# Optimization experiments

Measured on AMD Instinct MI355X. Metric: run time of the kernel, lower is better.

Reference implementation:

```python
import jax, jax.numpy as jnp
import numpy as np
from jax import lax

H = 1024        # hidden_size
V_IN = 32000    # input_size (source vocab)
V_OUT = 32000   # output_size (target vocab)
S = 128         # source sentence length
MAX_STEPS = 51  # decode loop bound (loop <= 50)
EOS = 2         # target_vocab['<eos>']


def _lstm_cell(x, h, c, W_ih, W_hh, b_ih, b_hh):
    # torch LSTMCell: gate order i, f, g, o
    gates = jnp.dot(W_ih, x) + b_ih + jnp.dot(W_hh, h) + b_hh  # [4H]
    i, f, g, o = jnp.split(gates, 4)
    i = jax.nn.sigmoid(i)
    f = jax.nn.sigmoid(f)
    g = jnp.tanh(g)
    o = jax.nn.sigmoid(o)
    c2 = f * c + i * g
    return o * jnp.tanh(c2), c2


def setup_inputs() -> dict:
    key = jax.random.key(0)
    ks = jax.random.split(key, 16)
    sc = 0.02
    p = {}
    p['src_ids'] = jax.random.randint(ks[0], (S,), 1, V_IN)
    emb_in = jax.random.normal(ks[1], (V_IN, H), jnp.float32) * sc
    p['embed_input'] = emb_in.at[0].set(0.0)  # padding_idx=0
    p['W_ih_e'] = jax.random.normal(ks[2], (4 * H, H), jnp.float32) * sc
    p['W_hh_e'] = jax.random.normal(ks[3], (4 * H, H), jnp.float32) * sc
    p['b_ih_e'] = jnp.zeros((4 * H,), jnp.float32)
    p['b_hh_e'] = jnp.zeros((4 * H,), jnp.float32)
    p['W_li'] = jax.random.normal(ks[4], (V_OUT, H), jnp.float32) * sc
    p['b_li'] = jnp.zeros((V_OUT,), jnp.float32)
    emb_t = jax.random.normal(ks[5], (V_OUT, H), jnp.float32) * sc
    p['embed_target'] = emb_t.at[0].set(0.0)  # padding_idx=0
    p['W_ih_d'] = jax.random.normal(ks[6], (4 * H, H), jnp.float32) * sc
    p['W_hh_d'] = jax.random.normal(ks[7], (4 * H, H), jnp.float32) * sc
    p['b_ih_d'] = jnp.zeros((4 * H,), jnp.float32)
    p['b_hh_d'] = jnp.zeros((4 * H,), jnp.float32)
    p['W_lt'] = jax.random.normal(ks[8], (V_OUT, H), jnp.float32) * sc
    p['b_lt'] = jnp.zeros((V_OUT,), jnp.float32)
    p['W_tl'] = jax.random.normal(ks[9], (H, 2 * H), jnp.float32) * sc
    p['b_tl'] = jnp.zeros((H,), jnp.float32)
    return p


def reference(src_ids, embed_input, W_ih_e, W_hh_e, b_ih_e, b_hh_e,
              W_li, b_li, embed_target, W_ih_d, W_hh_d, b_ih_d, b_hh_d,
              W_lt, b_lt, W_tl, b_tl):
    # ---- encoder: sequential LSTMCell over source tokens ----
    def enc_step(carry, tok):
        h, c = carry
        x = embed_input[tok]
        h2, c2 = _lstm_cell(x, h, c, W_ih_e, W_hh_e, b_ih_e, b_hh_e)
        return (h2, c2), h2

    h0 = jnp.zeros((H,), embed_input.dtype)
    (hs, cx), hs_all = lax.scan(enc_step, (h0, h0), src_ids)  # hs_all: [S,H]

    # first predicted word from final encoder state (argmax(softmax(z)) == argmax(z))
    wid0 = jnp.argmax(jnp.dot(W_li, hs) + b_li)
    tk0 = embed_target[wid0]
    ht, cx = _lstm_cell(tk0, hs, cx, W_ih_d, W_hh_d, b_ih_d, b_hh_d)

    # ---- greedy decode loop (fixed 51 steps, masked after <eos>) ----
    def dec_step(carry, _):
        wid, ht, cx, done = carry
        target_k = embed_target[wid]
        # dot-product attention over encoder states, softmax along source dim
        scores = jnp.dot(hs_all, ht)              # [S]
        a_t = jax.nn.softmax(scores)              # [S]
        d = jnp.dot(a_t, hs_all)                  # [H]
        concat = jnp.concatenate([d, ht])         # [2H]
        ht_new = jnp.tanh(jnp.dot(W_tl, concat) + b_tl)
        logits = jnp.dot(W_lt, ht_new) + b_lt     # [V_OUT]
        wid_new = jnp.argmax(logits)
        is_eos = wid_new == EOS
        out_tok = jnp.where(done | is_eos, -1, wid_new)  # -1 = not emitted
        ht2, cx2 = _lstm_cell(target_k, ht, cx, W_ih_d, W_hh_d, b_ih_d, b_hh_d)
        return (wid_new, ht2, cx2, done | is_eos), (out_tok, logits)

    done0 = wid0 == EOS
    _, (toks, logits) = lax.scan(dec_step, (wid0, ht, cx, done0), None, length=MAX_STEPS)
    return toks, logits  # toks: [51] emitted ids (-1 after eos), logits: [51, V_OUT]
```

## Files before the change

### kernel.cpp

```cpp
#include <hip/hip_runtime.h>
#include <float.h>
#include <math.h>

#define H      1024
#define SLEN   128
#define VOUT   32000
#define NSTEP  51
#define EOS_ID 2
#define NB     256
#define BT     1024
#define NWAVES 16
#define HROWS  4
#define LROWS  125
#define TOKS_OFF 51
#define QTAB_BYTES (LROWS*H)

typedef float fv4 __attribute__((ext_vector_type(4)));

struct Xch {
  unsigned long long h [2][H];
  unsigned long long ht[2][H];
  unsigned long long sc[2][SLEN];
  unsigned long long pv[2][NB];
};
__device__ Xch g_x;

__device__ __forceinline__ float wredsum(float v){
  v += __shfl_xor(v, 32, 64);
  v += __shfl_xor(v, 16, 64);
  v += __shfl_xor(v,  8, 64);
  v += __shfl_xor(v,  4, 64);
  v += __shfl_xor(v,  2, 64);
  v += __shfl_xor(v,  1, 64);
  return v;
}
__device__ __forceinline__ float wredmax(float v){
  v = fmaxf(v, __shfl_xor(v, 32, 64));
  v = fmaxf(v, __shfl_xor(v, 16, 64));
  v = fmaxf(v, __shfl_xor(v,  8, 64));
  v = fmaxf(v, __shfl_xor(v,  4, 64));
  v = fmaxf(v, __shfl_xor(v,  2, 64));
  v = fmaxf(v, __shfl_xor(v,  1, 64));
  return v;
}
__device__ __forceinline__ float sigm(float x){ return 1.0f/(1.0f+expf(-x)); }

__device__ __forceinline__ unsigned long long pollraw(const unsigned long long* p, unsigned tag){
  unsigned long long v = __hip_atomic_load(p, __ATOMIC_RELAXED, __HIP_MEMORY_SCOPE_AGENT);
  while((unsigned)(v & 0xffull) != tag){
    __builtin_amdgcn_s_sleep(1);
    v = __hip_atomic_load(p, __ATOMIC_RELAXED, __HIP_MEMORY_SCOPE_AGENT);
  }
  return v;
}
__device__ __forceinline__ float pollf(const unsigned long long* p, unsigned tag){
  return __uint_as_float((unsigned)(pollraw(p, tag) >> 32));
}
__device__ __forceinline__ void pubf(unsigned long long* p, float x, unsigned tag){
  __hip_atomic_store(p, (((unsigned long long)__float_as_uint(x))<<32) | (unsigned long long)tag,
                     __ATOMIC_RELAXED, __HIP_MEMORY_SCOPE_AGENT);
}
__device__ __forceinline__ void pubpv(unsigned long long* p, float v, int idx, unsigned tag){
  unsigned long long lo = (((unsigned long long)(unsigned)idx) << 8) | (unsigned long long)tag;
  __hip_atomic_store(p, (((unsigned long long)__float_as_uint(v))<<32) | lo,
                     __ATOMIC_RELAXED, __HIP_MEMORY_SCOPE_AGENT);
}

__device__ __forceinline__ float partdot(const float* __restrict__ a,
                                         const float* __restrict__ hp, int lane){
  const float4* a4 = (const float4*)a;
  const float4* h4 = (const float4*)hp;
  float s = 0.f;
#pragma unroll
  for(int k=0;k<4;k++){
    float4 x = a4[lane + 64*k];
    float4 y = h4[lane + 64*k];
    s = fmaf(x.x,y.x,s); s = fmaf(x.y,y.y,s);
    s = fmaf(x.z,y.z,s); s = fmaf(x.w,y.w,s);
  }
  return s;
}
__device__ __forceinline__ float partdot_nt(const float* __restrict__ a,
                                            const float* __restrict__ hp, int lane){
  const fv4* a4 = (const fv4*)a;
  const float4* h4 = (const float4*)hp;
  float s = 0.f;
#pragma unroll
  for(int k=0;k<4;k++){
    fv4 x = __builtin_nontemporal_load(a4 + lane + 64*k);
    float4 y = h4[lane + 64*k];
    s = fmaf(x.x,y.x,s); s = fmaf(x.y,y.y,s);
    s = fmaf(x.z,y.z,s); s = fmaf(x.w,y.w,s);
  }
  return s;
}

__device__ __forceinline__ float dotq(unsigned u, float4 hv, float acc){
  acc = fmaf((float)((int)(u<<24)>>24), hv.x, acc);
  acc = fmaf((float)((int)(u<<16)>>24), hv.y, acc);
  acc = fmaf((float)((int)(u<< 8)>>24), hv.z, acc);
  acc = fmaf((float)((int) u     >>24), hv.w, acc);
  return acc;
}

extern "C" __global__ void __launch_bounds__(BT)
nmt_kernel(const int* __restrict__ src_ids,
           const float* __restrict__ embed_input,
           const float* __restrict__ W_ih_e, const float* __restrict__ W_hh_e,
           const float* __restrict__ b_ih_e, const float* __restrict__ b_hh_e,
           const float* __restrict__ W_li,  const float* __restrict__ b_li,
           const float* __restrict__ embed_target,
           const float* __restrict__ W_ih_d, const float* __restrict__ W_hh_d,
           const float* __restrict__ b_ih_d, const float* __restrict__ b_hh_d,
           const float* __restrict__ W_lt,  const float* __restrict__ b_lt,
           const float* __restrict__ W_tl,  const float* __restrict__ b_tl,
           float* __restrict__ out)
{
  const int tid  = threadIdx.x;
  const int b    = blockIdx.x;
  const int w    = tid >> 6;
  const int lane = tid & 63;
  const int grow = (w>>2)*H + 4*b + (w&3);

  extern __shared__ __align__(16) char qmem[];
  uint4* qtab = (uint4*)qmem;

  __shared__ __align__(16) float hbuf[H];
  __shared__ __align__(16) float hsrow[H];
  __shared__ __align__(16) float htn_lds[H];
  __shared__ __align__(16) float xenc[SLEN][NWAVES];
  __shared__ __align__(16) float Mloc[HROWS][SLEN];
  __shared__ __align__(16) float sraw[SLEN];
  __shared__ __align__(16) float vloc[128];
  __shared__ __align__(16) float qrho[128];
  __shared__ __align__(16) float qinv[128];
  __shared__ __align__(16) float qbias[128];
  __shared__ int   rlist[128];
  __shared__ float gw4[4][4];
  __shared__ float c4[4];
  __shared__ float hn2[NWAVES];
  __shared__ float wred2[4];
  __shared__ float redv[NWAVES];
  __shared__ int   redi[NWAVES];
  __shared__ float gwhh_l[NWAVES];
  __shared__ int   wid_sh, done_sh;
  __shared__ float e_sh, rhomax_sh;
  __shared__ int   rcnt_sh;

#define PVPOLL47(TAG) do{                                                      \
    if(w>=4 && w<8){                                                           \
      unsigned long long v = pollraw(&g_x.pv[(TAG)&1][((w-4)<<6)+lane], (TAG));\
      float val = __uint_as_float((unsigned)(v>>32));                          \
      int   idx = (int)((unsigned)(v>>8) & 0xffffffu);                         \
      _Pragma("unroll")                                                        \
      for(int dd=32; dd>=1; dd>>=1){                                           \
        float ov=__shfl_xor(val,dd,64); int oi=__shfl_xor(idx,dd,64);          \
        if(ov>val || (ov==val && oi<idx)){ val=ov; idx=oi; }                   \
      }                                                                        \
      if(lane==0){ redv[w]=val; redi[w]=idx; }                                 \
    }                                                                          \
  }while(0)

  hbuf[tid] = 0.f;
  if(tid<4) c4[tid] = 0.f;
  __syncthreads();

  {
    const float4* wr = (const float4*)(W_ih_e + (size_t)grow*H);
    float4 w0=wr[lane], w1=wr[lane+64], w2=wr[lane+128], w3=wr[lane+192];
    const float bias = b_ih_e[grow] + b_hh_e[grow];
    for(int t=0;t<SLEN;t+=2){
      const float4* xr = (const float4*)(embed_input + (size_t)src_ids[t]*H);
      const float4* yr = (const float4*)(embed_input + (size_t)src_ids[t+1]*H);
      float4 x0=xr[lane], x1=xr[lane+64], x2=xr[lane+128], x3=xr[lane+192];
      float4 y0=yr[lane], y1=yr[lane+64], y2=yr[lane+128], y3=yr[lane+192];
      float s, u;
      s = w0.x*x0.x;        s = fmaf(w0.y,x0.y,s); s = fmaf(w0.z,x0.z,s); s = fmaf(w0.w,x0.w,s);
      u = w0.x*y0.x;        u = fmaf(w0.y,y0.y,u); u = fmaf(w0.z,y0.z,u); u = fmaf(w0.w,y0.w,u);
      s = fmaf(w1.x,x1.x,s); s = fmaf(w1.y,x1.y,s); s = fmaf(w1.z,x1.z,s); s = fmaf(w1.w,x1.w,s);
      u = fmaf(w1.x,y1.x,u); u = fmaf(w1.y,y1.y,u); u = fmaf(w1.z,y1.z,u); u = fmaf(w1.w,y1.w,u);
      s = fmaf(w2.x,x2.x,s); s = fmaf(w2.y,x2.y,s); s = fmaf(w2.z,x2.z,s); s = fmaf(w2.w,x2.w,s);
      u = fmaf(w2.x,y2.x,u); u = fmaf(w2.y,y2.y,u); u = fmaf(w2.z,y2.z,u); u = fmaf(w2.w,y2.w,u);
      s = fmaf(w3.x,x3.x,s); s = fmaf(w3.y,x3.y,s); s = fmaf(w3.w,x3.w,s); s = fmaf(w3.z,x3.z,s);
      u = fmaf(w3.x,y3.x,u); u = fmaf(w3.y,y3.y,u); u = fmaf(w3.w,y3.w,u); u = fmaf(w3.z,y3.z,u);
      s = wredsum(s); u = wredsum(u);
      if(lane==0){ xenc[t][w] = s + bias; xenc[t+1][w] = u + bias; }
    }
  }
  __syncthreads();

  for(int t=0;t<SLEN;t++){
    {
      float s = wredsum(partdot(W_hh_e + (size_t)grow*H, hbuf, lane)) + xenc[t][w];
      if(lane==0) gw4[w>>2][w&3] = s;
      if(w>=12 && t>0){
        float s2 = wredsum(partdot(W_tl + (size_t)(4*b+(w-12))*2*H, hbuf, lane));
        if(lane==0) Mloc[w-12][t-1]=s2;
      }
    }
    __syncthreads();
    if(tid<4){
      float gi=gw4[0][tid], gf=gw4[1][tid], gg=gw4[2][tid], go=gw4[3][tid];
      float ii=sigm(gi), ff=sigm(gf), g2=tanhf(gg), oo=sigm(go);
      float c2=fmaf(ff, c4[tid], ii*g2);
      c4[tid]=c2;
      pubf(&g_x.h[(t+1)&1][4*b+tid], oo*tanhf(c2), (unsigned)(t+1));
    }
    hbuf[tid] = pollf(&g_x.h[(t+1)&1][tid], (unsigned)(t+1));
    __syncthreads();
    if(b==t) hsrow[tid]=hbuf[tid];
  }
  if(w>=12){
    float s2 = wredsum(partdot(W_tl + (size_t)(4*b+(w-12))*2*H, hbuf, lane));
    if(lane==0) Mloc[w-12][SLEN-1]=s2;
  }
  __syncthreads();

  {
    const int rbase = b*LROWS;
#pragma unroll
    for(int t=0;t<8;t++){
      const int j = w + NWAVES*t;
      if(j < LROWS){
        const fv4* wr = (const fv4*)(W_lt + (size_t)(rbase+j)*H);
        fv4 g0=__builtin_nontemporal_load(wr+lane);
        fv4 g1=__builtin_nontemporal_load(wr+lane+64);
        fv4 g2=__builtin_nontemporal_load(wr+lane+128);
        fv4 g3=__builtin_nontemporal_load(wr+lane+192);
        float4 f0={g0.x,g0.y,g0.z,g0.w}, f1={g1.x,g1.y,g1.z,g1.w};
        float4 f2={g2.x,g2.y,g2.z,g2.w}, f3={g3.x,g3.y,g3.z,g3.w};
        float m;
        m = fmaxf(fabsf(f0.x),fabsf(f0.y)); m=fmaxf(m,fmaxf(fabsf(f0.z),fabsf(f0.w)));
        m = fmaxf(m,fmaxf(fabsf(f1.x),fabsf(f1.y))); m=fmaxf(m,fmaxf(fabsf(f1.z),fabsf(f1.w)));
        m = fmaxf(m,fmaxf(fabsf(f2.x),fabsf(f2.y))); m=fmaxf(m,fmaxf(fabsf(f2.z),fabsf(f2.w)));
        m = fmaxf(m,fmaxf(fabsf(f3.x),fabsf(f3.y))); m=fmaxf(m,fmaxf(fabsf(f3.z),fabsf(f3.w)));
        m = wredmax(m);
        const float s    = (m>1e-30f) ? 127.0f/m : 0.f;
        const float invs = (m>1e-30f) ? m*(1.0f/127.0f) : 0.f;
        float rsq = 0.f;
        unsigned pk[4];
        float4 ff[4] = {f0,f1,f2,f3};
#pragma unroll
        for(int u=0;u<4;u++){
          int q0=(int)rintf(ff[u].x*s), q1=(int)rintf(ff[u].y*s);
          int q2=(int)rintf(ff[u].z*s), q3=(int)rintf(ff[u].w*s);
          float d0=ff[u].x-(float)q0*invs, d1=ff[u].y-(float)q1*invs;
          float d2=ff[u].z-(float)q2*invs, d3=ff[u].w-(float)q3*invs;
          rsq=fmaf(d0,d0,rsq); rsq=fmaf(d1,d1,rsq);
          rsq=fmaf(d2,d2,rsq); rsq=fmaf(d3,d3,rsq);
          pk[u] = ((unsigned)(q0&255)) | ((unsigned)(q1&255)<<8)
                | ((unsigned)(q2&255)<<16) | ((unsigned)(q3&255)<<24);
        }
        uint4 qq; qq.x=pk[0]; qq.y=pk[1]; qq.z=pk[2]; qq.w=pk[3];
        qtab[j*64 + lane] = qq;
        rsq = wredsum(rsq);
        if(lane==0){
          qrho[j]  = sqrtf(rsq)*1.0002f + 1e-8f;
          qinv[j]  = invs;
          qbias[j] = b_lt[rbase+j];
        }
      }
    }
  }
  __syncthreads();
  {
    float rv = (tid<LROWS) ? qrho[tid] : 0.f;
    if(tid<128){
      float m = wredmax(rv);
      if(lane==0) wred2[w]=m;
    }
  }
  __syncthreads();
  if(tid==0) rhomax_sh = fmaxf(wred2[0], wred2[1]);

  {
    float bestv=-FLT_MAX; int besti=0;
    for(int j=w; j<LROWS; j+=NWAVES){
      const int r = b*LROWS + j;
      float s = wredsum(partdot_nt(W_li + (size_t)r*H, hbuf, lane));
      if(lane==0){
        float v = s + b_li[r];
        if(v>bestv){ bestv=v; besti=r; }
      }
    }
    if(lane==0){ redv[w]=bestv; redi[w]=besti; }
    __syncthreads();
    if(tid==0){
      float bv=redv[0]; int bi=redi[0];
      for(int i=1;i<NWAVES;i++)
        if(redv[i]>bv || (redv[i]==bv && redi[i]<bi)){ bv=redv[i]; bi=redi[i]; }
      pubpv(&g_x.pv[1][b], bv, bi, 1u);
    }
  }
  __syncthreads();
  PVPOLL47(1u);
  __syncthreads();
  if(tid==0){
    float bv=redv[4]; int bi=redi[4];
    for(int i=5;i<8;i++)
      if(redv[i]>bv || (redv[i]==bv && redi[i]<bi)){ bv=redv[i]; bi=redi[i]; }
    wid_sh = bi;
    done_sh = (bi==EOS_ID) ? 1 : 0;
  }
  __syncthreads();

  {
    const float* tk = embed_target + (size_t)wid_sh*H;
    float s = partdot(W_ih_d + (size_t)grow*H, tk, lane)
            + partdot(W_hh_d + (size_t)grow*H, hbuf, lane);
    s = wredsum(s);
    if(lane==0) gw4[w>>2][w&3] = s + b_ih_d[grow] + b_hh_d[grow];
  }
  __syncthreads();
  if(tid<4){
    float gi=gw4[0][tid], gf=gw4[1][tid], gg=gw4[2][tid], go=gw4[3][tid];
    float ii=sigm(gi), ff=sigm(gf), g2=tanhf(gg), oo=sigm(go);
    float c2=fmaf(ff, c4[tid], ii*g2);
    c4[tid]=c2;
    pubf(&g_x.h[1][4*b+tid], oo*tanhf(c2), 129u);
  }
  hbuf[tid] = pollf(&g_x.h[1][tid], 129u);
  __syncthreads();
  if(b<SLEN && w==0){
    float s = wredsum(partdot(hsrow, hbuf, lane));
    if(lane==0) pubf(&g_x.sc[1][b], s, 1u);
  }
  {
    float s=wredsum(partdot(W_hh_d + (size_t)grow*H, hbuf, lane));
    if(lane==0) gwhh_l[w]=s;
  }
  __syncthreads();

  for(int k=0;k<NSTEP;k++){
    const unsigned htag = (unsigned)(130+k);
    const unsigned ttag = (unsigned)(k+1);
    if(tid<SLEN) sraw[tid] = pollf(&g_x.sc[ttag&1][tid], ttag);
    __syncthreads();
    if(tid<SLEN){
      float m = wredmax(sraw[tid]);
      if(lane==0) wred2[w]=m;
    }
    __syncthreads();
    if(tid<SLEN){
      float mx=fmaxf(wred2[0],wred2[1]);
      float e=expf(sraw[tid]-mx);
      sraw[tid]=e;
      float z=wredsum(e);
      if(lane==0) wred2[2+w]=z;
    }
    __syncthreads();
    if(w<HROWS){
      const int r=4*b+w;
      float invZ=1.f/(wred2[2]+wred2[3]);
      float att=fmaf(sraw[2*lane],Mloc[w][2*lane], sraw[2*lane+1]*Mloc[w][2*lane+1]);
      float s=partdot(W_tl + (size_t)r*2*H + H, hbuf, lane);
      float tot=wredsum(fmaf(att,invZ,s));
      if(lane==0) pubf(&g_x.ht[ttag&1][r], tanhf(tot + b_tl[r]), ttag);
    }
    if(k>0) PVPOLL47(ttag);
    __syncthreads();
    if(k>0 && tid==0){
      float bv=redv[4]; int bi=redi[4];
      for(int i=5;i<8;i++)
        if(redv[i]>bv || (redv[i]==bv && redi[i]<bi)){ bv=redv[i]; bi=redi[i]; }
      int iseos=(bi==EOS_ID)?1:0;
      if(b==0) out[k-1]=(float)((done_sh|iseos)?-1:bi);
      done_sh |= iseos;
      wid_sh = bi;
    }
    __syncthreads();
    {
      const float* tk=embed_target + (size_t)wid_sh*H;
      float s=wredsum(partdot(W_ih_d + (size_t)grow*H, tk, lane));
      if(lane==0) gw4[w>>2][w&3] = s + gwhh_l[w] + b_ih_d[grow] + b_hh_d[grow];
    }
    __syncthreads();
    if(tid<4){
      float gi=gw4[0][tid], gf=gw4[1][tid], gg=gw4[2][tid], go=gw4[3][tid];
      float ii=sigm(gi), ff=sigm(gf), g2=tanhf(gg), oo=sigm(go);
      float c2=fmaf(ff, c4[tid], ii*g2);
      c4[tid]=c2;
      pubf(&g_x.h[htag&1][4*b+tid], oo*tanhf(c2), htag);
    }
    htn_lds[tid] = pollf(&g_x.ht[ttag&1][tid], ttag);
    __syncthreads();
    {
      float x = htn_lds[tid];
      float ss = wredsum(x*x);
      if(lane==0) hn2[w]=ss;
      if(tid==0) rcnt_sh=0;
    }
    __syncthreads();
    if(tid==0){
      float t2=0.f;
      for(int i=0;i<NWAVES;i++) t2+=hn2[i];
      float e = rhomax_sh * sqrtf(t2) * 1.0002f + 2e-3f;
      if(!(e>0.f && e<1e6f)) e=3.0e38f;
      e_sh = e;
    }
    {
      const float4* h4=(const float4*)htn_lds;
      float4 h0=h4[lane], h1=h4[lane+64], h2=h4[lane+128], h3=h4[lane+192];
#pragma unroll
      for(int t=0;t<8;t++){
        const int j=w+NWAVES*t;
        if(j<LROWS){
          uint4 q = qtab[j*64 + lane];
          float acc=0.f;
          acc=dotq(q.x,h0,acc); acc=dotq(q.y,h1,acc);
          acc=dotq(q.z,h2,acc); acc=dotq(q.w,h3,acc);
          acc=wredsum(acc);
          if(lane==0) vloc[j] = acc*qinv[j] + qbias[j];
        }
      }
    }
    __syncthreads();
    {
      const size_t obase = TOKS_OFF + (size_t)k*VOUT + (size_t)b*LROWS;
      if(tid<LROWS) out[obase+tid]=vloc[tid];
      float mv=(tid<LROWS)?vloc[tid]:-FLT_MAX;
      if(tid<128){
        float m=wredmax(mv);
        if(lane==0) wred2[w]=m;
      }
    }
    __syncthreads();
    {
      float thr = fmaxf(wred2[0],wred2[1]) - 2.0f*e_sh;
      if(tid<LROWS && vloc[tid]>=thr){
        int pos=atomicAdd(&rcnt_sh,1);
        rlist[pos]=tid;
      }
    }
    __syncthreads();
    hbuf[tid] = pollf(&g_x.h[htag&1][tid], htag);
    __syncthreads();
    if(b<SLEN && w==0){
      float s=wredsum(partdot(hsrow, hbuf, lane));
      if(lane==0) pubf(&g_x.sc[(k+2)&1][b], s, (unsigned)(k+2));
    }
    {
      float s=wredsum(partdot(W_hh_d + (size_t)grow*H, hbuf, lane));
      if(lane==0) gwhh_l[w]=s;
    }
    {
      float bestv=-FLT_MAX; int besti=0x7fffffff;
      const int nr=rcnt_sh;
      for(int s2=w;s2<nr;s2+=NWAVES){
        const int r=b*LROWS+rlist[s2];
        float s=wredsum(partdot_nt(W_lt + (size_t)r*H, htn_lds, lane));
        if(lane==0){
          float f=s+qbias[rlist[s2]];
          if(f>bestv || (f==bestv && r<besti)){ bestv=f; besti=r; }
        }
      }
      if(lane==0){ redv[w]=bestv; redi[w]=besti; }
    }
    __syncthreads();
    if(tid==0){
      float bv=redv[0]; int bi=redi[0];
      for(int i=1;i<NWAVES;i++)
        if(redv[i]>bv || (redv[i]==bv && redi[i]<bi)){ bv=redv[i]; bi=redi[i]; }
      pubpv(&g_x.pv[(k+2)&1][b], bv, bi, (unsigned)(k+2));
    }
  }

  if(b==0){
    PVPOLL47((unsigned)(NSTEP+1));
    __syncthreads();
    if(tid==0){
      float bv=redv[4]; int bi=redi[4];
      for(int i=5;i<8;i++)
        if(redv[i]>bv || (redv[i]==bv && redi[i]<bi)){ bv=redv[i]; bi=redi[i]; }
      int iseos=(bi==EOS_ID)?1:0;
      out[NSTEP-1]=(float)((done_sh|iseos)?-1:bi);
    }
  }
#undef PVPOLL47
}

extern "C" void kernel_launch(void* const* d_in, const int* in_sizes, int n_in,
                              void* d_out, int out_size, void* d_ws, size_t ws_size,
                              hipStream_t stream) {
  const int*   src_ids      = (const int*)  d_in[0];
  const float* embed_input  = (const float*)d_in[1];
  const float* W_ih_e       = (const float*)d_in[2];
  const float* W_hh_e       = (const float*)d_in[3];
  const float* b_ih_e       = (const float*)d_in[4];
  const float* b_hh_e       = (const float*)d_in[5];
  const float* W_li         = (const float*)d_in[6];
  const float* b_li         = (const float*)d_in[7];
  const float* embed_target = (const float*)d_in[8];
  const float* W_ih_d       = (const float*)d_in[9];
  const float* W_hh_d       = (const float*)d_in[10];
  const float* b_ih_d       = (const float*)d_in[11];
  const float* b_hh_d       = (const float*)d_in[12];
  const float* W_lt         = (const float*)d_in[13];
  const float* b_lt         = (const float*)d_in[14];
  const float* W_tl         = (const float*)d_in[15];
  const float* b_tl         = (const float*)d_in[16];
  float*       out          = (float*)d_out;

  void* sptr = nullptr;
  (void)hipGetSymbolAddress(&sptr, HIP_SYMBOL(g_x));
  if(sptr) (void)hipMemsetAsync(sptr, 0, sizeof(Xch), stream);

  void* args[] = {
    (void*)&src_ids, (void*)&embed_input,
    (void*)&W_ih_e, (void*)&W_hh_e, (void*)&b_ih_e, (void*)&b_hh_e,
    (void*)&W_li, (void*)&b_li, (void*)&embed_target,
    (void*)&W_ih_d, (void*)&W_hh_d, (void*)&b_ih_d, (void*)&b_hh_d,
    (void*)&W_lt, (void*)&b_lt, (void*)&W_tl, (void*)&b_tl,
    (void*)&out
  };

  hipError_t err = hipLaunchCooperativeKernel((const void*)nmt_kernel,
                                              dim3(NB), dim3(BT), args,
                                              QTAB_BYTES, stream);
  if (err != hipSuccess) {
    nmt_kernel<<<dim3(NB), dim3(BT), QTAB_BYTES, stream>>>(
        src_ids, embed_input, W_ih_e, W_hh_e, b_ih_e, b_hh_e,
        W_li, b_li, embed_target, W_ih_d, W_hh_d, b_ih_d, b_hh_d,
        W_lt, b_lt, W_tl, b_tl, out);
  }
}
```

Measured before the change: 2.258 ms.

## Run encoder and decoder LSTM on 64 blocks, overlap quantization on the rest

New measurement: 3.231 ms. 1.43x slower.

```diff
diff --git a/kernel.cpp b/kernel.cpp
--- a/kernel.cpp
+++ b/kernel.cpp
@@ -10,6 +10,8 @@
 #define NB     256
 #define BT     1024
 #define NWAVES 16
+#define NENC   64
+#define UPB    16
 #define HROWS  4
 #define LROWS  125
 #define TOKS_OFF 51
@@ -17,6 +19,7 @@
 
 typedef float fv4 __attribute__((ext_vector_type(4)));
 
+__device__ unsigned long long g_hs[SLEN][H];
 struct Xch {
   unsigned long long h [2][H];
   unsigned long long ht[2][H];
@@ -56,6 +59,10 @@
 __device__ __forceinline__ float pollf(const unsigned long long* p, unsigned tag){
   return __uint_as_float((unsigned)(pollraw(p, tag) >> 32));
 }
+__device__ __forceinline__ float loadpay(const unsigned long long* p){
+  return __uint_as_float((unsigned)(__hip_atomic_load(p, __ATOMIC_RELAXED,
+                                    __HIP_MEMORY_SCOPE_AGENT) >> 32));
+}
 __device__ __forceinline__ void pubf(unsigned long long* p, float x, unsigned tag){
   __hip_atomic_store(p, (((unsigned long long)__float_as_uint(x))<<32) | (unsigned long long)tag,
                      __ATOMIC_RELAXED, __HIP_MEMORY_SCOPE_AGENT);
@@ -77,6 +84,21 @@
     float4 y = h4[lane + 64*k];
     s = fmaf(x.x,y.x,s); s = fmaf(x.y,y.y,s);
     s = fmaf(x.z,y.z,s); s = fmaf(x.w,y.w,s);
+  }
+  return s;
+}
+__device__ __forceinline__ float partdot_g64(const float* __restrict__ a,
+                                             const unsigned long long* __restrict__ col,
+                                             int lane){
+  const float4* a4 = (const float4*)a;
+  float s = 0.f;
+#pragma unroll
+  for(int k=0;k<4;k++){
+    float4 x = a4[lane + 64*k];
+    const unsigned long long* cp = col + 4*(lane + 64*k);
+    float y0=loadpay(cp), y1=loadpay(cp+1), y2=loadpay(cp+2), y3=loadpay(cp+3);
+    s = fmaf(x.x,y0,s); s = fmaf(x.y,y1,s);
+    s = fmaf(x.z,y2,s); s = fmaf(x.w,y3,s);
   }
   return s;
 }
@@ -120,7 +142,7 @@
   const int b    = blockIdx.x;
   const int w    = tid >> 6;
   const int lane = tid & 63;
-  const int grow = (w>>2)*H + 4*b + (w&3);
+  const bool pub = (b < NENC);
 
   extern __shared__ __align__(16) char qmem[];
   uint4* qtab = (uint4*)qmem;
@@ -128,7 +150,6 @@
   __shared__ __align__(16) float hbuf[H];
   __shared__ __align__(16) float hsrow[H];
   __shared__ __align__(16) float htn_lds[H];
-  __shared__ __align__(16) float xenc[SLEN][NWAVES];
   __shared__ __align__(16) float Mloc[HROWS][SLEN];
   __shared__ __align__(16) float sraw[SLEN];
   __shared__ __align__(16) float vloc[128];
@@ -136,13 +157,13 @@
   __shared__ __align__(16) float qinv[128];
   __shared__ __align__(16) float qbias[128];
   __shared__ int   rlist[128];
-  __shared__ float gw4[4][4];
-  __shared__ float c4[4];
+  __shared__ float gw[4][UPB];
+  __shared__ float c16[UPB];
   __shared__ float hn2[NWAVES];
   __shared__ float wred2[4];
   __shared__ float redv[NWAVES];
   __shared__ int   redi[NWAVES];
-  __shared__ float gwhh_l[NWAVES];
+  __shared__ float gwhh_l[NWAVES][4];
   __shared__ int   wid_sh, done_sh;
   __shared__ float e_sh, rhomax_sh;
   __shared__ int   rcnt_sh;
@@ -161,62 +182,7 @@
     }                                                                          \
   }while(0)
 
-  hbuf[tid] = 0.f;
-  if(tid<4) c4[tid] = 0.f;
-  __syncthreads();
-
-  {
-    const float4* wr = (const float4*)(W_ih_e + (size_t)grow*H);
-    float4 w0=wr[lane], w1=wr[lane+64], w2=wr[lane+128], w3=wr[lane+192];
-    const float bias = b_ih_e[grow] + b_hh_e[grow];
-    for(int t=0;t<SLEN;t+=2){
-      const float4* xr = (const float4*)(embed_input + (size_t)src_ids[t]*H);
-      const float4* yr = (const float4*)(embed_input + (size_t)src_ids[t+1]*H);
-      float4 x0=xr[lane], x1=xr[lane+64], x2=xr[lane+128], x3=xr[lane+192];
-      float4 y0=yr[lane], y1=yr[lane+64], y2=yr[lane+128], y3=yr[lane+192];
-      float s, u;
-      s = w0.x*x0.x;        s = fmaf(w0.y,x0.y,s); s = fmaf(w0.z,x0.z,s); s = fmaf(w0.w,x0.w,s);
-      u = w0.x*y0.x;        u = fmaf(w0.y,y0.y,u); u = fmaf(w0.z,y0.z,u); u = fmaf(w0.w,y0.w,u);
-      s = fmaf(w1.x,x1.x,s); s = fmaf(w1.y,x1.y,s); s = fmaf(w1.z,x1.z,s); s = fmaf(w1.w,x1.w,s);
-      u = fmaf(w1.x,y1.x,u); u = fmaf(w1.y,y1.y,u); u = fmaf(w1.z,y1.z,u); u = fmaf(w1.w,y1.w,u);
-      s = fmaf(w2.x,x2.x,s); s = fmaf(w2.y,x2.y,s); s = fmaf(w2.z,x2.z,s); s = fmaf(w2.w,x2.w,s);
-      u = fmaf(w2.x,y2.x,u); u = fmaf(w2.y,y2.y,u); u = fmaf(w2.z,y2.z,u); u = fmaf(w2.w,y2.w,u);
-      s = fmaf(w3.x,x3.x,s); s = fmaf(w3.y,x3.y,s); s = fmaf(w3.w,x3.w,s); s = fmaf(w3.z,x3.z,s);
-      u = fmaf(w3.x,y3.x,u); u = fmaf(w3.y,y3.y,u); u = fmaf(w3.w,y3.w,u); u = fmaf(w3.z,y3.z,u);
-      s = wredsum(s); u = wredsum(u);
-      if(lane==0){ xenc[t][w] = s + bias; xenc[t+1][w] = u + bias; }
-    }
-  }
-  __syncthreads();
-
-  for(int t=0;t<SLEN;t++){
-    {
-      float s = wredsum(partdot(W_hh_e + (size_t)grow*H, hbuf, lane)) + xenc[t][w];
-      if(lane==0) gw4[w>>2][w&3] = s;
-      if(w>=12 && t>0){
-        float s2 = wredsum(partdot(W_tl + (size_t)(4*b+(w-12))*2*H, hbuf, lane));
-        if(lane==0) Mloc[w-12][t-1]=s2;
-      }
-    }
-    __syncthreads();
-    if(tid<4){
-      float gi=gw4[0][tid], gf=gw4[1][tid], gg=gw4[2][tid], go=gw4[3][tid];
-      float ii=sigm(gi), ff=sigm(gf), g2=tanhf(gg), oo=sigm(go);
-      float c2=fmaf(ff, c4[tid], ii*g2);
-      c4[tid]=c2;
-      pubf(&g_x.h[(t+1)&1][4*b+tid], oo*tanhf(c2), (unsigned)(t+1));
-    }
-    hbuf[tid] = pollf(&g_x.h[(t+1)&1][tid], (unsigned)(t+1));
-    __syncthreads();
-    if(b==t) hsrow[tid]=hbuf[tid];
-  }
-  if(w>=12){
-    float s2 = wredsum(partdot(W_tl + (size_t)(4*b+(w-12))*2*H, hbuf, lane));
-    if(lane==0) Mloc[w-12][SLEN-1]=s2;
-  }
-  __syncthreads();
-
-  {
+  auto do_quant = [&](){
     const int rbase = b*LROWS;
 #pragma unroll
     for(int t=0;t<8;t++){
@@ -261,17 +227,113 @@
         }
       }
     }
-  }
+    __syncthreads();
+    {
+      float rv = (tid<LROWS) ? qrho[tid] : 0.f;
+      if(tid<128){
+        float m = wredmax(rv);
+        if(lane==0) wred2[w]=m;
+      }
+    }
+    __syncthreads();
+    if(tid==0) rhomax_sh = fmaxf(wred2[0], wred2[1]);
+    __syncthreads();
+  };
+
+  hbuf[tid] = 0.f;
+  if(tid<UPB) c16[tid] = 0.f;
   __syncthreads();
-  {
-    float rv = (tid<LROWS) ? qrho[tid] : 0.f;
-    if(tid<128){
-      float m = wredmax(rv);
-      if(lane==0) wred2[w]=m;
-    }
-  }
-  __syncthreads();
-  if(tid==0) rhomax_sh = fmaxf(wred2[0], wred2[1]);
+
+  if(pub){
+    float xv0[4], xv1[4];
+#pragma unroll
+    for(int i=0;i<4;i++){
+      const int row = (w>>2)*H + UPB*b + 4*(w&3) + i;
+      const float4* wr = (const float4*)(W_ih_e + (size_t)row*H);
+      float4 w0=wr[lane], w1=wr[lane+64], w2=wr[lane+128], w3=wr[lane+192];
+      const float bias = b_ih_e[row] + b_hh_e[row];
+      for(int t=0;t<SLEN;t+=2){
+        const float4* xr = (const float4*)(embed_input + (size_t)src_ids[t]*H);
+        const float4* yr = (const float4*)(embed_input + (size_t)src_ids[t+1]*H);
+        float4 x0=xr[lane], x1=xr[lane+64], x2=xr[lane+128], x3=xr[lane+192];
+        float4 y0=yr[lane], y1=yr[lane+64], y2=yr[lane+128], y3=yr[lane+192];
+        float s, u;
+        s = w0.x*x0.x;        s = fmaf(w0.y,x0.y,s); s = fmaf(w0.z,x0.z,s); s = fmaf(w0.w,x0.w,s);
+        u = w0.x*y0.x;        u = fmaf(w0.y,y0.y,u); u = fmaf(w0.z,y0.z,u); u = fmaf(w0.w,y0.w,u);
+        s = fmaf(w1.x,x1.x,s); s = fmaf(w1.y,x1.y,s); s = fmaf(w1.z,x1.z,s); s = fmaf(w1.w,x1.w,s);
+        u = fmaf(w1.x,y1.x,u); u = fmaf(w1.y,y1.y,u); u = fmaf(w1.z,y1.z,u); u = fmaf(w1.w,y1.w,u);
+        s = fmaf(w2.x,x2.x,s); s = fmaf(w2.y,x2.y,s); s = fmaf(w2.z,x2.z,s); s = fmaf(w2.w,x2.w,s);
+        u = fmaf(w2.x,y2.x,u); u = fmaf(w2.y,y2.y,u); u = fmaf(w2.z,y2.z,u); u = fmaf(w2.w,y2.w,u);
+        s = fmaf(w3.x,x3.x,s); s = fmaf(w3.y,x3.y,s); s = fmaf(w3.w,x3.w,s); s = fmaf(w3.z,x3.z,s);
+        u = fmaf(w3.x,y3.x,u); u = fmaf(w3.y,y3.y,u); u = fmaf(w3.w,y3.w,u); u = fmaf(w3.z,y3.z,u);
+        s = wredsum(s); u = wredsum(u);
+        if(t < 64){
+          if(lane==(t&63))     xv0[i] = s + bias;
+          if(lane==((t+1)&63)) xv0[i] = u + bias;
+        }else{
+          if(lane==(t&63))     xv1[i] = s + bias;
+          if(lane==((t+1)&63)) xv1[i] = u + bias;
+        }
+      }
+    }
+    __syncthreads();
+
+    for(int t=0;t<SLEN;t++){
+      float sg[4];
+#pragma unroll
+      for(int i=0;i<4;i++){
+        const int row = (w>>2)*H + UPB*b + 4*(w&3) + i;
+        sg[i] = wredsum(partdot(W_hh_e + (size_t)row*H, hbuf, lane));
+      }
+#pragma unroll
+      for(int i=0;i<4;i++){
+        float xh = (t<64) ? xv0[i] : xv1[i];
+        float xi = __shfl(xh, t&63, 64);
+        if(lane==0) gw[w>>2][4*(w&3)+i] = sg[i] + xi;
+      }
+      __syncthreads();
+      if(tid<UPB){
+        float gi=gw[0][tid], gf=gw[1][tid], gg=gw[2][tid], go=gw[3][tid];
+        float ii=sigm(gi), ff=sigm(gf), g2=tanhf(gg), oo=sigm(go);
+        float c2=fmaf(ff, c16[tid], ii*g2);
+        c16[tid]=c2;
+        pubf(&g_hs[t][UPB*b+tid], oo*tanhf(c2), (unsigned)(t+1));
+      }
+      hbuf[tid] = pollf(&g_hs[t][tid], (unsigned)(t+1));
+      __syncthreads();
+    }
+    hsrow[tid] = loadpay(&g_hs[b][tid]);
+    {
+      const int r = w&3, c0 = (w>>2)*32;
+      for(int cc=0;cc<32;cc++){
+        const int col = c0+cc;
+        float s = wredsum(partdot_g64(W_tl + (size_t)(4*b+r)*2*H, g_hs[col], lane));
+        if(lane==0) Mloc[r][col]=s;
+      }
+    }
+    __syncthreads();
+    do_quant();
+  } else {
+    do_quant();
+    for(int c=0;c<16;c++){
+      const int tl = 8*c+7;
+      unsigned long long sv = pollraw(&g_hs[tl][tid], (unsigned)(tl+1));
+      for(int cc=0;cc<8;cc++){
+        const int col = 8*c+cc;
+        float hv;
+        if(cc<7) hv = loadpay(&g_hs[col][tid]);
+        else     hv = __uint_as_float((unsigned)(sv>>32));
+        hbuf[tid]=hv;
+        __syncthreads();
+        if(b==col) hsrow[tid]=hbuf[tid];
+        if(w<HROWS){
+          float s2 = wredsum(partdot(W_tl + (size_t)(4*b+w)*2*H, hbuf, lane));
+          if(lane==0) Mloc[w][col]=s2;
+        }
+        __syncthreads();
+      }
+    }
+  }
 
   {
     float bestv=-FLT_MAX; int besti=0;
@@ -304,20 +366,24 @@
   }
   __syncthreads();
 
-  {
+  if(pub){
     const float* tk = embed_target + (size_t)wid_sh*H;
-    float s = partdot(W_ih_d + (size_t)grow*H, tk, lane)
-            + partdot(W_hh_d + (size_t)grow*H, hbuf, lane);
-    s = wredsum(s);
-    if(lane==0) gw4[w>>2][w&3] = s + b_ih_d[grow] + b_hh_d[grow];
+#pragma unroll
+    for(int i=0;i<4;i++){
+      const int row = (w>>2)*H + UPB*b + 4*(w&3) + i;
+      float s = partdot(W_ih_d + (size_t)row*H, tk, lane)
+              + partdot(W_hh_d + (size_t)row*H, hbuf, lane);
+      s = wredsum(s);
+      if(lane==0) gw[w>>2][4*(w&3)+i] = s + b_ih_d[row] + b_hh_d[row];
+    }
   }
   __syncthreads();
-  if(tid<4){
-    float gi=gw4[0][tid], gf=gw4[1][tid], gg=gw4[2][tid], go=gw4[3][tid];
+  if(pub && tid<UPB){
+    float gi=gw[0][tid], gf=gw[1][tid], gg=gw[2][tid], go=gw[3][tid];
     float ii=sigm(gi), ff=sigm(gf), g2=tanhf(gg), oo=sigm(go);
-    float c2=fmaf(ff, c4[tid], ii*g2);
-    c4[tid]=c2;
-    pubf(&g_x.h[1][4*b+tid], oo*tanhf(c2), 129u);
+    float c2=fmaf(ff, c16[tid], ii*g2);
+    c16[tid]=c2;
+    pubf(&g_x.h[1][UPB*b+tid], oo*tanhf(c2), 129u);
   }
   hbuf[tid] = pollf(&g_x.h[1][tid], 129u);
   __syncthreads();
@@ -325,9 +391,13 @@
     float s = wredsum(partdot(hsrow, hbuf, lane));
     if(lane==0) pubf(&g_x.sc[1][b], s, 1u);
   }
-  {
-    float s=wredsum(partdot(W_hh_d + (size_t)grow*H, hbuf, lane));
-    if(lane==0) gwhh_l[w]=s;
+  if(pub){
+#pragma unroll
+    for(int i=0;i<4;i++){
+      const int row = (w>>2)*H + UPB*b + 4*(w&3) + i;
+      float s=wredsum(partdot(W_hh_d + (size_t)row*H, hbuf, lane));
+      if(lane==0) gwhh_l[w][i]=s;
+    }
   }
   __syncthreads();
 
@@ -369,18 +439,22 @@
       wid_sh = bi;
     }
     __syncthreads();
-    {
+    if(pub){
       const float* tk=embed_target + (size_t)wid_sh*H;
-      float s=wredsum(partdot(W_ih_d + (size_t)grow*H, tk, lane));
-      if(lane==0) gw4[w>>2][w&3] = s + gwhh_l[w] + b_ih_d[grow] + b_hh_d[grow];
-    }
-    __syncthreads();
-    if(tid<4){
-      float gi=gw4[0][tid], gf=gw4[1][tid], gg=gw4[2][tid], go=gw4[3][tid];
+#pragma unroll
+      for(int i=0;i<4;i++){
+        const int row = (w>>2)*H + UPB*b + 4*(w&3) + i;
+        float s=wredsum(partdot(W_ih_d + (size_t)row*H, tk, lane));
+        if(lane==0) gw[w>>2][4*(w&3)+i] = s + gwhh_l[w][i] + b_ih_d[row] + b_hh_d[row];
+      }
+    }
+    __syncthreads();
+    if(pub && tid<UPB){
+      float gi=gw[0][tid], gf=gw[1][tid], gg=gw[2][tid], go=gw[3][tid];
       float ii=sigm(gi), ff=sigm(gf), g2=tanhf(gg), oo=sigm(go);
-      float c2=fmaf(ff, c4[tid], ii*g2);
-      c4[tid]=c2;
-      pubf(&g_x.h[htag&1][4*b+tid], oo*tanhf(c2), htag);
+      float c2=fmaf(ff, c16[tid], ii*g2);
+      c16[tid]=c2;
+      pubf(&g_x.h[htag&1][UPB*b+tid], oo*tanhf(c2), htag);
     }
     htn_lds[tid] = pollf(&g_x.ht[ttag&1][tid], ttag);
     __syncthreads();
@@ -439,9 +513,13 @@
       float s=wredsum(partdot(hsrow, hbuf, lane));
       if(lane==0) pubf(&g_x.sc[(k+2)&1][b], s, (unsigned)(k+2));
     }
-    {
-      float s=wredsum(partdot(W_hh_d + (size_t)grow*H, hbuf, lane));
-      if(lane==0) gwhh_l[w]=s;
+    if(pub){
+#pragma unroll
+      for(int i=0;i<4;i++){
+        const int row = (w>>2)*H + UPB*b + 4*(w&3) + i;
+        float s=wredsum(partdot(W_hh_d + (size_t)row*H, hbuf, lane));
+        if(lane==0) gwhh_l[w][i]=s;
+      }
     }
     {
       float bestv=-FLT_MAX; int besti=0x7fffffff;
@@ -504,6 +582,9 @@
   void* sptr = nullptr;
   (void)hipGetSymbolAddress(&sptr, HIP_SYMBOL(g_x));
   if(sptr) (void)hipMemsetAsync(sptr, 0, sizeof(Xch), stream);
+  void* hptr = nullptr;
+  (void)hipGetSymbolAddress(&hptr, HIP_SYMBOL(g_hs));
+  if(hptr) (void)hipMemsetAsync(hptr, 0, sizeof(unsigned long long)*SLEN*H, stream);
 
   void* args[] = {
     (void*)&src_ids, (void*)&embed_input,
```

## Split persistent kernel into separate encoder and decoder cooperative kernels

Applied to the files above, without the earlier changes.

Measured after the change: 2.184 ms. 1.03x faster.

```diff
diff --git a/kernel.cpp b/kernel.cpp
--- a/kernel.cpp
+++ b/kernel.cpp
@@ -24,6 +24,8 @@
   unsigned long long pv[2][NB];
 };
 __device__ Xch g_x;
+__device__ __align__(16) float g_hsall[SLEN][H];
+__device__ __align__(16) float g_c[H];
 
 __device__ __forceinline__ float wredsum(float v){
   v += __shfl_xor(v, 32, 64);
@@ -104,17 +106,10 @@
 }
 
 extern "C" __global__ void __launch_bounds__(BT)
-nmt_kernel(const int* __restrict__ src_ids,
-           const float* __restrict__ embed_input,
-           const float* __restrict__ W_ih_e, const float* __restrict__ W_hh_e,
-           const float* __restrict__ b_ih_e, const float* __restrict__ b_hh_e,
-           const float* __restrict__ W_li,  const float* __restrict__ b_li,
-           const float* __restrict__ embed_target,
-           const float* __restrict__ W_ih_d, const float* __restrict__ W_hh_d,
-           const float* __restrict__ b_ih_d, const float* __restrict__ b_hh_d,
-           const float* __restrict__ W_lt,  const float* __restrict__ b_lt,
-           const float* __restrict__ W_tl,  const float* __restrict__ b_tl,
-           float* __restrict__ out)
+nmt_enc(const int* __restrict__ src_ids,
+        const float* __restrict__ embed_input,
+        const float* __restrict__ W_ih_e, const float* __restrict__ W_hh_e,
+        const float* __restrict__ b_ih_e, const float* __restrict__ b_hh_e)
 {
   const int tid  = threadIdx.x;
   const int b    = blockIdx.x;
@@ -122,44 +117,10 @@
   const int lane = tid & 63;
   const int grow = (w>>2)*H + 4*b + (w&3);
 
-  extern __shared__ __align__(16) char qmem[];
-  uint4* qtab = (uint4*)qmem;
-
   __shared__ __align__(16) float hbuf[H];
-  __shared__ __align__(16) float hsrow[H];
-  __shared__ __align__(16) float htn_lds[H];
   __shared__ __align__(16) float xenc[SLEN][NWAVES];
-  __shared__ __align__(16) float Mloc[HROWS][SLEN];
-  __shared__ __align__(16) float sraw[SLEN];
-  __shared__ __align__(16) float vloc[128];
-  __shared__ __align__(16) float qrho[128];
-  __shared__ __align__(16) float qinv[128];
-  __shared__ __align__(16) float qbias[128];
-  __shared__ int   rlist[128];
   __shared__ float gw4[4][4];
   __shared__ float c4[4];
-  __shared__ float hn2[NWAVES];
-  __shared__ float wred2[4];
-  __shared__ float redv[NWAVES];
-  __shared__ int   redi[NWAVES];
-  __shared__ float gwhh_l[NWAVES];
-  __shared__ int   wid_sh, done_sh;
-  __shared__ float e_sh, rhomax_sh;
-  __shared__ int   rcnt_sh;
-
-#define PVPOLL47(TAG) do{                                                      \
-    if(w>=4 && w<8){                                                           \
-      unsigned long long v = pollraw(&g_x.pv[(TAG)&1][((w-4)<<6)+lane], (TAG));\
-      float val = __uint_as_float((unsigned)(v>>32));                          \
-      int   idx = (int)((unsigned)(v>>8) & 0xffffffu);                         \
-      _Pragma("unroll")                                                        \
-      for(int dd=32; dd>=1; dd>>=1){                                           \
-        float ov=__shfl_xor(val,dd,64); int oi=__shfl_xor(idx,dd,64);          \
-        if(ov>val || (ov==val && oi<idx)){ val=ov; idx=oi; }                   \
-      }                                                                        \
-      if(lane==0){ redv[w]=val; redi[w]=idx; }                                 \
-    }                                                                          \
-  }while(0)
 
   hbuf[tid] = 0.f;
   if(tid<4) c4[tid] = 0.f;
@@ -193,10 +154,6 @@
     {
       float s = wredsum(partdot(W_hh_e + (size_t)grow*H, hbuf, lane)) + xenc[t][w];
       if(lane==0) gw4[w>>2][w&3] = s;
-      if(w>=12 && t>0){
-        float s2 = wredsum(partdot(W_tl + (size_t)(4*b+(w-12))*2*H, hbuf, lane));
-        if(lane==0) Mloc[w-12][t-1]=s2;
-      }
     }
     __syncthreads();
     if(tid<4){
@@ -208,11 +165,75 @@
     }
     hbuf[tid] = pollf(&g_x.h[(t+1)&1][tid], (unsigned)(t+1));
     __syncthreads();
-    if(b==t) hsrow[tid]=hbuf[tid];
-  }
-  if(w>=12){
-    float s2 = wredsum(partdot(W_tl + (size_t)(4*b+(w-12))*2*H, hbuf, lane));
-    if(lane==0) Mloc[w-12][SLEN-1]=s2;
+    if(b==t) g_hsall[t][tid] = hbuf[tid];
+  }
+  if(tid<4) g_c[4*b+tid] = c4[tid];
+}
+
+extern "C" __global__ void __launch_bounds__(BT)
+nmt_dec(const float* __restrict__ W_li,  const float* __restrict__ b_li,
+        const float* __restrict__ embed_target,
+        const float* __restrict__ W_ih_d, const float* __restrict__ W_hh_d,
+        const float* __restrict__ b_ih_d, const float* __restrict__ b_hh_d,
+        const float* __restrict__ W_lt,  const float* __restrict__ b_lt,
+        const float* __restrict__ W_tl,  const float* __restrict__ b_tl,
+        float* __restrict__ out)
+{
+  const int tid  = threadIdx.x;
+  const int b    = blockIdx.x;
+  const int w    = tid >> 6;
+  const int lane = tid & 63;
+  const int grow = (w>>2)*H + 4*b + (w&3);
+
+  extern __shared__ __align__(16) char qmem[];
+  uint4* qtab = (uint4*)qmem;
+
+  __shared__ __align__(16) float hbuf[H];
+  __shared__ __align__(16) float hsrow[H];
+  __shared__ __align__(16) float htn_lds[H];
+  __shared__ __align__(16) float Mloc[HROWS][SLEN];
+  __shared__ __align__(16) float sraw[SLEN];
+  __shared__ __align__(16) float vloc[128];
+  __shared__ __align__(16) float qrho[128];
+  __shared__ __align__(16) float qinv[128];
+  __shared__ __align__(16) float qbias[128];
+  __shared__ int   rlist[128];
+  __shared__ float gw4[4][4];
+  __shared__ float c4[4];
+  __shared__ float hn2[NWAVES];
+  __shared__ float wred2[4];
+  __shared__ float redv[NWAVES];
+  __shared__ int   redi[NWAVES];
+  __shared__ float gwhh_l[NWAVES];
+  __shared__ int   wid_sh, done_sh;
+  __shared__ float e_sh, rhomax_sh;
+  __shared__ int   rcnt_sh;
+
+#define PVPOLL47(TAG) do{                                                      \
+    if(w>=4 && w<8){                                                           \
+      unsigned long long v = pollraw(&g_x.pv[(TAG)&1][((w-4)<<6)+lane], (TAG));\
+      float val = __uint_as_float((unsigned)(v>>32));                          \
+      int   idx = (int)((unsigned)(v>>8) & 0xffffffu);                         \
+      _Pragma("unroll")                                                        \
+      for(int dd=32; dd>=1; dd>>=1){                                           \
+        float ov=__shfl_xor(val,dd,64); int oi=__shfl_xor(idx,dd,64);          \
+        if(ov>val || (ov==val && oi<idx)){ val=ov; idx=oi; }                   \
+      }                                                                        \
+      if(lane==0){ redv[w]=val; redi[w]=idx; }                                 \
+    }                                                                          \
+  }while(0)
+
+  hbuf[tid] = g_hsall[SLEN-1][tid];
+  if(b<SLEN) hsrow[tid] = g_hsall[b][tid];
+  if(tid<4)  c4[tid] = g_c[4*b+tid];
+  __syncthreads();
+  {
+    const int r = w&3, cbase = (w>>2)*32;
+    for(int cc=0;cc<32;cc++){
+      const int col = cbase+cc;
+      float s = wredsum(partdot(W_tl + (size_t)(4*b+r)*2*H, g_hsall[col], lane));
+      if(lane==0) Mloc[r][col]=s;
+    }
   }
   __syncthreads();
 
@@ -505,21 +526,28 @@
   (void)hipGetSymbolAddress(&sptr, HIP_SYMBOL(g_x));
   if(sptr) (void)hipMemsetAsync(sptr, 0, sizeof(Xch), stream);
 
-  void* args[] = {
+  void* argsA[] = {
     (void*)&src_ids, (void*)&embed_input,
-    (void*)&W_ih_e, (void*)&W_hh_e, (void*)&b_ih_e, (void*)&b_hh_e,
+    (void*)&W_ih_e, (void*)&W_hh_e, (void*)&b_ih_e, (void*)&b_hh_e
+  };
+  hipError_t e1 = hipLaunchCooperativeKernel((const void*)nmt_enc,
+                                             dim3(NB), dim3(BT), argsA, 0, stream);
+  if (e1 != hipSuccess) {
+    nmt_enc<<<dim3(NB), dim3(BT), 0, stream>>>(
+        src_ids, embed_input, W_ih_e, W_hh_e, b_ih_e, b_hh_e);
+  }
+
+  void* argsB[] = {
     (void*)&W_li, (void*)&b_li, (void*)&embed_target,
     (void*)&W_ih_d, (void*)&W_hh_d, (void*)&b_ih_d, (void*)&b_hh_d,
     (void*)&W_lt, (void*)&b_lt, (void*)&W_tl, (void*)&b_tl,
     (void*)&out
   };
-
-  hipError_t err = hipLaunchCooperativeKernel((const void*)nmt_kernel,
-                                              dim3(NB), dim3(BT), args,
-                                              QTAB_BYTES, stream);
-  if (err != hipSuccess) {
-    nmt_kernel<<<dim3(NB), dim3(BT), QTAB_BYTES, stream>>>(
-        src_ids, embed_input, W_ih_e, W_hh_e, b_ih_e, b_hh_e,
+  hipError_t e2 = hipLaunchCooperativeKernel((const void*)nmt_dec,
+                                             dim3(NB), dim3(BT), argsB,
+                                             QTAB_BYTES, stream);
+  if (e2 != hipSuccess) {
+    nmt_dec<<<dim3(NB), dim3(BT), QTAB_BYTES, stream>>>(
         W_li, b_li, embed_target, W_ih_d, W_hh_d, b_ih_d, b_hh_d,
         W_lt, b_lt, W_tl, b_tl, out);
   }
```
